# Performance work log

Measured on AMD Instinct MI355X. Metric: run time of the kernel, lower is better.

## Reference

```python
import jax, jax.numpy as jnp
import numpy as np

N_NODES = 50000
N_EDGES = 800000
N_GRAPHS = 256
W_SCALE = 0.05  # keep activations bounded through 5 relu conv layers


def setup_inputs() -> dict:
    key = jax.random.key(0)
    ks = jax.random.split(key, 16)
    rn = lambda k, shape: W_SCALE * jax.random.normal(k, shape, dtype=jnp.float32)
    return {
        "x": jax.random.normal(ks[0], (N_NODES, 336), dtype=jnp.float32),
        "edge_index": jax.random.randint(ks[1], (2, N_EDGES), 0, N_NODES, dtype=jnp.int32),
        "batch": jnp.sort(jax.random.randint(ks[2], (N_NODES,), 0, N_GRAPHS, dtype=jnp.int32)),
        "w1_rel": rn(ks[3], (100, 336)),
        "w1_root": rn(ks[4], (100, 336)),
        "b1": rn(ks[5], (100,)),
        "w_rel": rn(ks[6], (4, 100, 100)),
        "w_root": rn(ks[7], (4, 100, 100)),
        "b": rn(ks[8], (4, 100)),
        "lw1": rn(ks[9], (100, 100)),
        "lb1": rn(ks[10], (100,)),
        "lw2": rn(ks[11], (100, 100)),
        "lb2": rn(ks[12], (100,)),
        "lw3": rn(ks[13], (29, 100)),
        "lb3": rn(ks[14], (29,)),
    }


def _graph_conv(x, edge_index, w_rel, w_root, bias):
    # PyG GraphConv: out_i = W_rel @ (sum_{j->i} x_j) + b + W_root @ x_i
    src, dst = edge_index[0], edge_index[1]
    agg = jax.ops.segment_sum(x[src], dst, num_segments=x.shape[0])  # [N, d_in]
    return agg @ w_rel.T + bias + x @ w_root.T


def reference(x, edge_index, batch, w1_rel, w1_root, b1, w_rel, w_root, b,
              lw1, lb1, lw2, lb2, lw3, lb3):
    h = jax.nn.relu(_graph_conv(x, edge_index, w1_rel, w1_root, b1))  # [N,100]
    for i in range(4):  # conv2..conv5 (structurally distinct params)
        h = jax.nn.relu(_graph_conv(h, edge_index, w_rel[i], w_root[i], b[i]))
    # global_mean_pool over graphs
    sums = jax.ops.segment_sum(h, batch, num_segments=N_GRAPHS)          # [G,100]
    counts = jax.ops.segment_sum(jnp.ones((h.shape[0],), h.dtype), batch,
                                 num_segments=N_GRAPHS)                  # [G]
    pooled = sums / jnp.maximum(counts, 1.0)[:, None]
    h = jax.nn.relu(pooled @ lw1.T + lb1)
    h = jax.nn.relu(h @ lw2.T + lb2)
    return h @ lw3.T + lb3  # [G, 29]
```

## Files before the change

kernel.cpp:

```cpp
#include <hip/hip_runtime.h>

#define N_NODES 50000
#define N_EDGES 800000
#define N_GRAPHS 256
#define F 100

#define SCAN_B 512
#define SCAN_NB 98
#define SCAN_PAD (SCAN_NB * SCAN_B)

#define PART_SZ 6250
#define FILL_CHUNK 2048

typedef __attribute__((ext_vector_type(8))) short bf16x8;
typedef __attribute__((ext_vector_type(4))) float f32x4;
typedef unsigned short ushort_t;
typedef unsigned int uint_t;

__device__ inline ushort_t f2bf(float f) {
  uint_t u = __float_as_uint(f);
  uint_t r = (u + 0x7fffu + ((u >> 16) & 1u)) >> 16;
  return (ushort_t)r;
}


__global__ __launch_bounds__(256) void hist_kernel(const int* __restrict__ dst,
                                                   int* __restrict__ cnt, int E) {
  int part = blockIdx.x & 7;
  int lo = part * PART_SZ, hi = lo + PART_SZ;
  int base = (blockIdx.x >> 3) * FILL_CHUNK;
  int end = base + FILL_CHUNK; if (end > E) end = E;
  for (int i = base + threadIdx.x; i < end; i += 256) {
    int d = dst[i];
    if (d >= lo && d < hi) atomicAdd(&cnt[d], 1);
  }
}

__global__ __launch_bounds__(SCAN_B) void scan1_kernel(const int* __restrict__ cnt,
                                                       int* __restrict__ excl,
                                                       int* __restrict__ bsum) {
  __shared__ int sh[SCAN_B];
  int t = threadIdx.x;
  int i = blockIdx.x * SCAN_B + t;
  int v = cnt[i];
  sh[t] = v;
  __syncthreads();
  for (int off = 1; off < SCAN_B; off <<= 1) {
    int u = (t >= off) ? sh[t - off] : 0;
    __syncthreads();
    sh[t] += u;
    __syncthreads();
  }
  excl[i] = sh[t] - v;
  if (t == SCAN_B - 1) bsum[blockIdx.x] = sh[t];
}

__global__ __launch_bounds__(128) void scan2_kernel(int* __restrict__ bsum) {
  __shared__ int sh[128];
  int t = threadIdx.x;
  int v = (t < SCAN_NB) ? bsum[t] : 0;
  sh[t] = v;
  __syncthreads();
  for (int off = 1; off < 128; off <<= 1) {
    int u = (t >= off) ? sh[t - off] : 0;
    __syncthreads();
    sh[t] += u;
    __syncthreads();
  }
  if (t < SCAN_NB) bsum[t] = sh[t] - v;
}

__global__ __launch_bounds__(SCAN_B) void scan3_kernel(const int* __restrict__ excl,
                                                       const int* __restrict__ bsum,
                                                       int* __restrict__ offs,
                                                       int* __restrict__ cursor) {
  int i = blockIdx.x * SCAN_B + threadIdx.x;
  int v = excl[i] + bsum[blockIdx.x];
  if (i <= N_NODES) { offs[i] = v; cursor[i] = v; }
}

__global__ __launch_bounds__(256) void fill_kernel(const int* __restrict__ src,
                                                   const int* __restrict__ dst,
                                                   int* __restrict__ cursor,
                                                   int* __restrict__ csr_src, int E) {
  int part = blockIdx.x & 7;
  int lo = part * PART_SZ, hi = lo + PART_SZ;
  int base = (blockIdx.x >> 3) * FILL_CHUNK;
  int end = base + FILL_CHUNK; if (end > E) end = E;
  for (int i = base + threadIdx.x; i < end; i += 256) {
    int d = dst[i];
    if (d >= lo && d < hi) {
      int p = atomicAdd(&cursor[d], 1);
      csr_src[p] = src[i];
    }
  }
}


__global__ void pack_w1_kernel(const float* __restrict__ w1_rel, const float* __restrict__ w1_root,
                               ushort_t* __restrict__ Wp1) {
  int row = blockIdx.x;
  for (int k = threadIdx.x; k < 352; k += 128) {
    float v = 0.f;
    if (k < 336) {
      if (row < 100) v = w1_rel[row * 336 + k];
      else if (row < 200) v = w1_root[(row - 100) * 336 + k];
    }
    Wp1[(size_t)row * 352 + k] = f2bf(v);
  }
}

__global__ void pack_w_kernel(const float* __restrict__ w_rel, const float* __restrict__ w_root,
                              ushort_t* __restrict__ Wp) {
  int row = blockIdx.x;
  int l = blockIdx.y;
  int k = threadIdx.x;
  float v = 0.f;
  if (k < 100) {
    if (row < 100) v = w_rel[((size_t)l * 100 + row) * 100 + k];
    else if (row < 200) v = w_root[((size_t)l * 100 + row - 100) * 100 + k];
  }
  Wp[((size_t)l * 208 + row) * 128 + k] = f2bf(v);
}


template <bool AF32>
__global__ __launch_bounds__(256) void conv_mfma(
    const void* __restrict__ Aptr, const ushort_t* __restrict__ Wp,
    const float* __restrict__ bias,
    ushort_t* __restrict__ Zrel, ushort_t* __restrict__ Zroot, int Kp) {
  __shared__ short alds[64 * 32];
  __shared__ short blds[208 * 32];
  __shared__ float bias_s[104];

  int tid = threadIdx.x;
  int n0 = blockIdx.x * 64;
  if (tid < 100) bias_s[tid] = bias[tid];

  f32x4 acc[13];
#pragma unroll
  for (int b = 0; b < 13; ++b) acc[b] = (f32x4)0.f;

  int w = tid >> 6, lane = tid & 63, q = lane >> 4, m16 = lane & 15;

  for (int k0 = 0; k0 < Kp; k0 += 32) {
    {
      int r = tid >> 2, qq = tid & 3;
      int node = n0 + r;
      int k = k0 + qq * 8;
      bf16x8 val = (bf16x8)0;
      if (AF32) {
        if (node < N_NODES && k < 336) {
          const float* p = (const float*)Aptr + (size_t)node * 336 + k;
          float4 f0 = *(const float4*)p;
          float4 f1 = *(const float4*)(p + 4);
          val[0] = (short)f2bf(f0.x); val[1] = (short)f2bf(f0.y);
          val[2] = (short)f2bf(f0.z); val[3] = (short)f2bf(f0.w);
          val[4] = (short)f2bf(f1.x); val[5] = (short)f2bf(f1.y);
          val[6] = (short)f2bf(f1.z); val[7] = (short)f2bf(f1.w);
        }
      } else {
        if (node < N_NODES)
          val = *(const bf16x8*)((const short*)Aptr + (size_t)node * 128 + k);
      }
      *(bf16x8*)&alds[r * 32 + qq * 8] = val;
    }
    for (int c = tid; c < 832; c += 256) {
      int r = c >> 2, qq = c & 3;
      *(bf16x8*)&blds[r * 32 + qq * 8] =
          *(const bf16x8*)((const short*)Wp + (size_t)r * Kp + k0 + qq * 8);
    }
    __syncthreads();
    bf16x8 a = *(const bf16x8*)&alds[(w * 16 + m16) * 32 + q * 8];
#pragma unroll
    for (int b = 0; b < 13; ++b) {
      bf16x8 bf = *(const bf16x8*)&blds[(b * 16 + m16) * 32 + q * 8];
      acc[b] = __builtin_amdgcn_mfma_f32_16x16x32_bf16(a, bf, acc[b], 0, 0, 0);
    }
    __syncthreads();
  }

  int node_base = n0 + w * 16 + q * 4;
#pragma unroll
  for (int b = 0; b < 13; ++b) {
    int n = b * 16 + m16;
#pragma unroll
    for (int r = 0; r < 4; ++r) {
      int node = node_base + r;
      if (node >= N_NODES) continue;
      float v = acc[b][r];
      if (n < 100) {
        Zrel[(size_t)node * 100 + n] = f2bf(v);
      } else if (n < 200) {
        Zroot[(size_t)node * 100 + (n - 100)] = f2bf(v + bias_s[n - 100]);
      }
    }
  }
}


__global__ __launch_bounds__(256) void gather_bf16(
    const ushort_t* __restrict__ Zrel, const ushort_t* __restrict__ Zroot,
    const int* __restrict__ offs, const int* __restrict__ csr,
    ushort_t* __restrict__ H) {
  int node = blockIdx.x * 4 + (threadIdx.x >> 6);
  node = __builtin_amdgcn_readfirstlane(node);
  int lane = threadIdx.x & 63;
  int off = (lane < 50 ? lane : 49) * 2;

  uint_t z = *(const uint_t*)(Zroot + (size_t)node * 100 + off);
  float p0[8], p1[8];
#pragma unroll
  for (int u = 0; u < 8; ++u) { p0[u] = 0.f; p1[u] = 0.f; }
  p0[0] = __uint_as_float(z << 16);
  p1[0] = __uint_as_float(z & 0xffff0000u);

  int s = offs[node], e = offs[node + 1];
  int j = s;
  for (; j + 7 < e; j += 8) {
    uint_t zz[8];
#pragma unroll
    for (int u = 0; u < 8; ++u) {
      int idx = csr[j + u];
      zz[u] = *(const uint_t*)(Zrel + (size_t)idx * 100 + off);
    }
#pragma unroll
    for (int u = 0; u < 8; ++u) {
      p0[u] += __uint_as_float(zz[u] << 16);
      p1[u] += __uint_as_float(zz[u] & 0xffff0000u);
    }
  }
  for (; j < e; ++j) {
    int idx = csr[j];
    uint_t z0 = *(const uint_t*)(Zrel + (size_t)idx * 100 + off);
    p0[0] += __uint_as_float(z0 << 16);
    p1[0] += __uint_as_float(z0 & 0xffff0000u);
  }
  float a0 = ((p0[0] + p0[1]) + (p0[2] + p0[3])) + ((p0[4] + p0[5]) + (p0[6] + p0[7]));
  float a1 = ((p1[0] + p1[1]) + (p1[2] + p1[3])) + ((p1[4] + p1[5]) + (p1[6] + p1[7]));
  a0 = fmaxf(a0, 0.f);
  a1 = fmaxf(a1, 0.f);
  uint_t outp = (uint_t)f2bf(a0) | ((uint_t)f2bf(a1) << 16);
  if (lane >= 50) outp = 0u;
  *(uint_t*)(H + (size_t)node * 128 + lane * 2) = outp;
}


__global__ __launch_bounds__(1024) void pool_kernel(const ushort_t* __restrict__ H,
                                                    const int* __restrict__ batch,
                                                    float* __restrict__ pooled) {
  int g = blockIdx.x;
  int t = threadIdx.x;
  int lo = 0, hi = N_NODES;
  while (lo < hi) { int mid = (lo + hi) >> 1; if (batch[mid] < g) lo = mid + 1; else hi = mid; }
  int s = lo;
  hi = N_NODES;
  while (lo < hi) { int mid = (lo + hi) >> 1; if (batch[mid] <= g) lo = mid + 1; else hi = mid; }
  int e = lo;

  int row = t >> 6;
  int lane = t & 63;
  int off = (lane < 50 ? lane : 49) * 2;
  float a0 = 0.f, a1 = 0.f;
  for (int n = s + row; n < e; n += 16) {
    uint_t z = *(const uint_t*)(H + (size_t)n * 128 + off);
    a0 += __uint_as_float(z << 16);
    a1 += __uint_as_float(z & 0xffff0000u);
  }
  __shared__ float sh[16][104];
  if (lane < 50) { sh[row][lane * 2] = a0; sh[row][lane * 2 + 1] = a1; }
  __syncthreads();
  if (t < 100) {
    float acc = 0.f;
#pragma unroll
    for (int r = 0; r < 16; ++r) acc += sh[r][t];
    int cnt = e - s;
    float d = (cnt > 0) ? (float)cnt : 1.f;
    pooled[(size_t)g * F + t] = acc / d;
  }
}


__global__ void mlp_kernel(const float* __restrict__ pooled,
                           const float* __restrict__ lw1, const float* __restrict__ lb1,
                           const float* __restrict__ lw2, const float* __restrict__ lb2,
                           const float* __restrict__ lw3, const float* __restrict__ lb3,
                           float* __restrict__ out) {
  int g = blockIdx.x;
  int t = threadIdx.x;
  __shared__ float r0[F], r1[F], r2[F];
  if (t < F) r0[t] = pooled[(size_t)g * F + t];
  __syncthreads();
  if (t < F) {
    float s = lb1[t];
    for (int k = 0; k < F; ++k) s += r0[k] * lw1[t * F + k];
    r1[t] = fmaxf(s, 0.f);
  }
  __syncthreads();
  if (t < F) {
    float s = lb2[t];
    for (int k = 0; k < F; ++k) s += r1[k] * lw2[t * F + k];
    r2[t] = fmaxf(s, 0.f);
  }
  __syncthreads();
  if (t < 29) {
    float s = lb3[t];
    for (int k = 0; k < F; ++k) s += r2[k] * lw3[t * F + k];
    out[g * 29 + t] = s;
  }
}


extern "C" void kernel_launch(void* const* d_in, const int* in_sizes, int n_in,
                              void* d_out, int out_size, void* d_ws, size_t ws_size,
                              hipStream_t stream) {
  const float* x       = (const float*)d_in[0];
  const int*   ei      = (const int*)d_in[1];
  const int*   batch   = (const int*)d_in[2];
  const float* w1_rel  = (const float*)d_in[3];
  const float* w1_root = (const float*)d_in[4];
  const float* b1      = (const float*)d_in[5];
  const float* w_rel   = (const float*)d_in[6];
  const float* w_root  = (const float*)d_in[7];
  const float* bvec    = (const float*)d_in[8];
  const float* lw1     = (const float*)d_in[9];
  const float* lb1     = (const float*)d_in[10];
  const float* lw2     = (const float*)d_in[11];
  const float* lb2     = (const float*)d_in[12];
  const float* lw3     = (const float*)d_in[13];
  const float* lb3     = (const float*)d_in[14];
  float* out = (float*)d_out;

  char* ws = (char*)d_ws;
  size_t o = 0;
  auto alloc = [&](size_t bytes) { void* p = ws + o; o = (o + bytes + 511) & ~(size_t)511; return p; };
  ushort_t* H    = (ushort_t*)alloc((size_t)N_NODES * 128 * 2);
  ushort_t* Zrel = (ushort_t*)alloc((size_t)N_NODES * 100 * 2);
  ushort_t* Zroot= (ushort_t*)alloc((size_t)N_NODES * 100 * 2);
  ushort_t* Wp1  = (ushort_t*)alloc((size_t)208 * 352 * 2);
  ushort_t* Wp   = (ushort_t*)alloc((size_t)4 * 208 * 128 * 2);
  float*    pooled = (float*)alloc((size_t)N_GRAPHS * F * 4);
  int* cnt    = (int*)alloc((size_t)SCAN_PAD * 4);
  int* excl   = (int*)alloc((size_t)SCAN_PAD * 4);
  int* bsum   = (int*)alloc((size_t)128 * 4);
  int* offs   = (int*)alloc((size_t)(N_NODES + 1) * 4);
  int* cursor = (int*)alloc((size_t)(N_NODES + 1) * 4);
  int* csr    = (int*)alloc((size_t)N_EDGES * 4);

  const int E = N_EDGES;
  const int* srcv = ei;
  const int* dstv = ei + E;

  int nchunk = (E + FILL_CHUNK - 1) / FILL_CHUNK;
  hipMemsetAsync(cnt, 0, (size_t)SCAN_PAD * sizeof(int), stream);
  hist_kernel<<<nchunk * 8, 256, 0, stream>>>(dstv, cnt, E);
  scan1_kernel<<<SCAN_NB, SCAN_B, 0, stream>>>(cnt, excl, bsum);
  scan2_kernel<<<1, 128, 0, stream>>>(bsum);
  scan3_kernel<<<SCAN_NB, SCAN_B, 0, stream>>>(excl, bsum, offs, cursor);
  fill_kernel<<<nchunk * 8, 256, 0, stream>>>(srcv, dstv, cursor, csr, E);

  pack_w1_kernel<<<208, 128, 0, stream>>>(w1_rel, w1_root, Wp1);
  pack_w_kernel<<<dim3(208, 4), 128, 0, stream>>>(w_rel, w_root, Wp);

  int mmgrid = (N_NODES + 63) / 64;
  conv_mfma<true><<<mmgrid, 256, 0, stream>>>(x, Wp1, b1, Zrel, Zroot, 352);
  gather_bf16<<<N_NODES / 4, 256, 0, stream>>>(Zrel, Zroot, offs, csr, H);
  for (int l = 0; l < 4; ++l) {
    conv_mfma<false><<<mmgrid, 256, 0, stream>>>(H, Wp + (size_t)l * 208 * 128,
                                                 bvec + (size_t)l * F, Zrel, Zroot, 128);
    gather_bf16<<<N_NODES / 4, 256, 0, stream>>>(Zrel, Zroot, offs, csr, H);
  }
  pool_kernel<<<N_GRAPHS, 1024, 0, stream>>>(H, batch, pooled);
  mlp_kernel<<<N_GRAPHS, 128, 0, stream>>>(pooled, lw1, lb1, lw2, lb2, lw3, lb3, out);
}
```

Before: 475.7 us.

## Double-buffer conv GEMM K-chunks in registers, widen to 64, unroll gather by 16

The conv MFMA kernel now works on 64-wide K chunks and prefetches the next chunk's A and B tiles into registers while MFMAs run on the current LDS tile. It also pads LDS rows to 72 shorts to reduce bank conflicts, and pads the first-layer weight to K=384 to fit the new chunk size. The gather kernel issues 16 independent neighbour loads per iteration plus a 4-wide tail, to expose more memory-level parallelism. The cost is more registers, which may lower occupancy, plus some extra zero-padded K work in layer 1.

```diff
diff --git a/kernel.cpp b/kernel.cpp
--- a/kernel.cpp
+++ b/kernel.cpp
@@ -11,6 +11,8 @@
 
 #define PART_SZ 6250
 #define FILL_CHUNK 2048
+
+#define SROW 72
 
 typedef __attribute__((ext_vector_type(8))) short bf16x8;
 typedef __attribute__((ext_vector_type(4))) float f32x4;
@@ -100,13 +102,13 @@
 __global__ void pack_w1_kernel(const float* __restrict__ w1_rel, const float* __restrict__ w1_root,
                                ushort_t* __restrict__ Wp1) {
   int row = blockIdx.x;
-  for (int k = threadIdx.x; k < 352; k += 128) {
+  for (int k = threadIdx.x; k < 384; k += 128) {
     float v = 0.f;
     if (k < 336) {
       if (row < 100) v = w1_rel[row * 336 + k];
       else if (row < 200) v = w1_root[(row - 100) * 336 + k];
     }
-    Wp1[(size_t)row * 352 + k] = f2bf(v);
+    Wp1[(size_t)row * 384 + k] = f2bf(v);
   }
 }
 
@@ -129,8 +131,8 @@
     const void* __restrict__ Aptr, const ushort_t* __restrict__ Wp,
     const float* __restrict__ bias,
     ushort_t* __restrict__ Zrel, ushort_t* __restrict__ Zroot, int Kp) {
-  __shared__ short alds[64 * 32];
-  __shared__ short blds[208 * 32];
+  __shared__ short alds[64 * SROW];
+  __shared__ short blds[208 * SROW];
   __shared__ float bias_s[104];
 
   int tid = threadIdx.x;
@@ -143,11 +145,17 @@
 
   int w = tid >> 6, lane = tid & 63, q = lane >> 4, m16 = lane & 15;
 
-  for (int k0 = 0; k0 < Kp; k0 += 32) {
-    {
-      int r = tid >> 2, qq = tid & 3;
-      int node = n0 + r;
-      int k = k0 + qq * 8;
+  int ar[2], aq[2];
+#pragma unroll
+  for (int u = 0; u < 2; ++u) { int c = tid + u * 256; ar[u] = c >> 3; aq[u] = c & 7; }
+
+  bf16x8 areg[2], breg[7];
+
+  auto load_chunk = [&](int k0) {
+#pragma unroll
+    for (int u = 0; u < 2; ++u) {
+      int node = n0 + ar[u];
+      int k = k0 + aq[u] * 8;
       bf16x8 val = (bf16x8)0;
       if (AF32) {
         if (node < N_NODES && k < 336) {
@@ -163,19 +171,42 @@
         if (node < N_NODES)
           val = *(const bf16x8*)((const short*)Aptr + (size_t)node * 128 + k);
       }
-      *(bf16x8*)&alds[r * 32 + qq * 8] = val;
-    }
-    for (int c = tid; c < 832; c += 256) {
-      int r = c >> 2, qq = c & 3;
-      *(bf16x8*)&blds[r * 32 + qq * 8] =
-          *(const bf16x8*)((const short*)Wp + (size_t)r * Kp + k0 + qq * 8);
-    }
-    __syncthreads();
-    bf16x8 a = *(const bf16x8*)&alds[(w * 16 + m16) * 32 + q * 8];
-#pragma unroll
-    for (int b = 0; b < 13; ++b) {
-      bf16x8 bf = *(const bf16x8*)&blds[(b * 16 + m16) * 32 + q * 8];
-      acc[b] = __builtin_amdgcn_mfma_f32_16x16x32_bf16(a, bf, acc[b], 0, 0, 0);
+      areg[u] = val;
+    }
+#pragma unroll
+    for (int u = 0; u < 7; ++u) {
+      int c = tid + u * 256;
+      if (c < 1664) {
+        int r = c >> 3, qq = c & 7;
+        breg[u] = *(const bf16x8*)((const short*)Wp + (size_t)r * Kp + k0 + qq * 8);
+      }
+    }
+  };
+
+  load_chunk(0);
+
+  for (int k0 = 0; k0 < Kp; k0 += 64) {
+#pragma unroll
+    for (int u = 0; u < 2; ++u)
+      *(bf16x8*)&alds[ar[u] * SROW + aq[u] * 8] = areg[u];
+#pragma unroll
+    for (int u = 0; u < 7; ++u) {
+      int c = tid + u * 256;
+      if (c < 1664) {
+        int r = c >> 3, qq = c & 7;
+        *(bf16x8*)&blds[r * SROW + qq * 8] = breg[u];
+      }
+    }
+    __syncthreads();
+    if (k0 + 64 < Kp) load_chunk(k0 + 64);
+#pragma unroll
+    for (int s = 0; s < 2; ++s) {
+      bf16x8 a = *(const bf16x8*)&alds[(w * 16 + m16) * SROW + s * 32 + q * 8];
+#pragma unroll
+      for (int b = 0; b < 13; ++b) {
+        bf16x8 bf = *(const bf16x8*)&blds[(b * 16 + m16) * SROW + s * 32 + q * 8];
+        acc[b] = __builtin_amdgcn_mfma_f32_16x16x32_bf16(a, bf, acc[b], 0, 0, 0);
+      }
     }
     __syncthreads();
   }
@@ -217,15 +248,28 @@
 
   int s = offs[node], e = offs[node + 1];
   int j = s;
-  for (; j + 7 < e; j += 8) {
-    uint_t zz[8];
-#pragma unroll
-    for (int u = 0; u < 8; ++u) {
+  for (; j + 15 < e; j += 16) {
+    uint_t zz[16];
+#pragma unroll
+    for (int u = 0; u < 16; ++u) {
       int idx = csr[j + u];
       zz[u] = *(const uint_t*)(Zrel + (size_t)idx * 100 + off);
     }
 #pragma unroll
-    for (int u = 0; u < 8; ++u) {
+    for (int u = 0; u < 16; ++u) {
+      p0[u & 7] += __uint_as_float(zz[u] << 16);
+      p1[u & 7] += __uint_as_float(zz[u] & 0xffff0000u);
+    }
+  }
+  for (; j + 3 < e; j += 4) {
+    uint_t zz[4];
+#pragma unroll
+    for (int u = 0; u < 4; ++u) {
+      int idx = csr[j + u];
+      zz[u] = *(const uint_t*)(Zrel + (size_t)idx * 100 + off);
+    }
+#pragma unroll
+    for (int u = 0; u < 4; ++u) {
       p0[u] += __uint_as_float(zz[u] << 16);
       p1[u] += __uint_as_float(zz[u] & 0xffff0000u);
     }
@@ -337,7 +381,7 @@
   ushort_t* H    = (ushort_t*)alloc((size_t)N_NODES * 128 * 2);
   ushort_t* Zrel = (ushort_t*)alloc((size_t)N_NODES * 100 * 2);
   ushort_t* Zroot= (ushort_t*)alloc((size_t)N_NODES * 100 * 2);
-  ushort_t* Wp1  = (ushort_t*)alloc((size_t)208 * 352 * 2);
+  ushort_t* Wp1  = (ushort_t*)alloc((size_t)208 * 384 * 2);
   ushort_t* Wp   = (ushort_t*)alloc((size_t)4 * 208 * 128 * 2);
   float*    pooled = (float*)alloc((size_t)N_GRAPHS * F * 4);
   int* cnt    = (int*)alloc((size_t)SCAN_PAD * 4);
@@ -363,7 +407,7 @@
   pack_w_kernel<<<dim3(208, 4), 128, 0, stream>>>(w_rel, w_root, Wp);
 
   int mmgrid = (N_NODES + 63) / 64;
-  conv_mfma<true><<<mmgrid, 256, 0, stream>>>(x, Wp1, b1, Zrel, Zroot, 352);
+  conv_mfma<true><<<mmgrid, 256, 0, stream>>>(x, Wp1, b1, Zrel, Zroot, 384);
   gather_bf16<<<N_NODES / 4, 256, 0, stream>>>(Zrel, Zroot, offs, csr, H);
   for (int l = 0; l < 4; ++l) {
     conv_mfma<false><<<mmgrid, 256, 0, stream>>>(H, Wp + (size_t)l * 208 * 128,
```

Result: no change. 468.3 us (-1.6%).

## Split conv GEMM over output halves, drop LDS staging, widen gather to 128-padded rows

Applied to the files above, without the earlier changes.

The conv GEMM now splits the 224 padded output columns into two grid halves of 112. It loads A and W fragments directly from global memory into MFMA operands, with the K loop fully unrolled, instead of staging them through LDS with barriers. Zrel and Zroot are padded to 128-element rows. The gather kernel loads a wave's 64 CSR indices at once, broadcasts them with readlane, and has each half-wave process a different neighbor with 8-byte loads, then combines the halves with a shuffle. The aim is to remove LDS and sync overhead and to raise memory-level parallelism in the edge gather. The cost is redundant global A loads across the two halves and more padded bytes.

```diff
diff --git a/kernel.cpp b/kernel.cpp
--- a/kernel.cpp
+++ b/kernel.cpp
@@ -12,6 +12,8 @@
 #define PART_SZ 6250
 #define FILL_CHUNK 2048
 
+#define NBH 112
+
 typedef __attribute__((ext_vector_type(8))) short bf16x8;
 typedef __attribute__((ext_vector_type(4))) float f32x4;
 typedef unsigned short ushort_t;
@@ -22,6 +24,8 @@
   uint_t r = (u + 0x7fffu + ((u >> 16) & 1u)) >> 16;
   return (ushort_t)r;
 }
+__device__ inline float bflo(uint_t u) { return __uint_as_float(u << 16); }
+__device__ inline float bfhi(uint_t u) { return __uint_as_float(u & 0xffff0000u); }
 
 
 __global__ __launch_bounds__(256) void hist_kernel(const int* __restrict__ dst,
@@ -120,79 +124,68 @@
     if (row < 100) v = w_rel[((size_t)l * 100 + row) * 100 + k];
     else if (row < 200) v = w_root[((size_t)l * 100 + row - 100) * 100 + k];
   }
-  Wp[((size_t)l * 208 + row) * 128 + k] = f2bf(v);
-}
-
-
-template <bool AF32>
+  Wp[((size_t)l * 224 + row) * 128 + k] = f2bf(v);
+}
+
+
+template <bool AF32, int NS>
 __global__ __launch_bounds__(256) void conv_mfma(
     const void* __restrict__ Aptr, const ushort_t* __restrict__ Wp,
     const float* __restrict__ bias,
     ushort_t* __restrict__ Zrel, ushort_t* __restrict__ Zroot, int Kp) {
-  __shared__ short alds[64 * 32];
-  __shared__ short blds[208 * 32];
-  __shared__ float bias_s[104];
-
   int tid = threadIdx.x;
+  int w = tid >> 6, lane = tid & 63, q = lane >> 4, m16 = lane & 15;
   int n0 = blockIdx.x * 64;
-  if (tid < 100) bias_s[tid] = bias[tid];
-
-  f32x4 acc[13];
-#pragma unroll
-  for (int b = 0; b < 13; ++b) acc[b] = (f32x4)0.f;
-
-  int w = tid >> 6, lane = tid & 63, q = lane >> 4, m16 = lane & 15;
-
-  for (int k0 = 0; k0 < Kp; k0 += 32) {
-    {
-      int r = tid >> 2, qq = tid & 3;
-      int node = n0 + r;
-      int k = k0 + qq * 8;
+  int h = blockIdx.y;
+  int arow = n0 + w * 16 + m16;
+  int arow_c = arow < N_NODES ? arow : N_NODES - 1;
+
+  f32x4 acc[7];
+#pragma unroll
+  for (int b = 0; b < 7; ++b) acc[b] = (f32x4)0.f;
+
+  const ushort_t* wbase = Wp + (size_t)(h * NBH) * Kp;
+
+#pragma unroll
+  for (int s = 0; s < NS; ++s) {
+    int base = s * 32 + q * 8;
+    bf16x8 a;
+    if (AF32) {
       bf16x8 val = (bf16x8)0;
-      if (AF32) {
-        if (node < N_NODES && k < 336) {
-          const float* p = (const float*)Aptr + (size_t)node * 336 + k;
-          float4 f0 = *(const float4*)p;
-          float4 f1 = *(const float4*)(p + 4);
-          val[0] = (short)f2bf(f0.x); val[1] = (short)f2bf(f0.y);
-          val[2] = (short)f2bf(f0.z); val[3] = (short)f2bf(f0.w);
-          val[4] = (short)f2bf(f1.x); val[5] = (short)f2bf(f1.y);
-          val[6] = (short)f2bf(f1.z); val[7] = (short)f2bf(f1.w);
-        }
-      } else {
-        if (node < N_NODES)
-          val = *(const bf16x8*)((const short*)Aptr + (size_t)node * 128 + k);
+      if (base < 336) {
+        const float* p = (const float*)Aptr + (size_t)arow_c * 336 + base;
+        float4 f0 = *(const float4*)p;
+        float4 f1 = *(const float4*)(p + 4);
+        val[0] = (short)f2bf(f0.x); val[1] = (short)f2bf(f0.y);
+        val[2] = (short)f2bf(f0.z); val[3] = (short)f2bf(f0.w);
+        val[4] = (short)f2bf(f1.x); val[5] = (short)f2bf(f1.y);
+        val[6] = (short)f2bf(f1.z); val[7] = (short)f2bf(f1.w);
       }
-      *(bf16x8*)&alds[r * 32 + qq * 8] = val;
-    }
-    for (int c = tid; c < 832; c += 256) {
-      int r = c >> 2, qq = c & 3;
-      *(bf16x8*)&blds[r * 32 + qq * 8] =
-          *(const bf16x8*)((const short*)Wp + (size_t)r * Kp + k0 + qq * 8);
-    }
-    __syncthreads();
-    bf16x8 a = *(const bf16x8*)&alds[(w * 16 + m16) * 32 + q * 8];
-#pragma unroll
-    for (int b = 0; b < 13; ++b) {
-      bf16x8 bf = *(const bf16x8*)&blds[(b * 16 + m16) * 32 + q * 8];
+      a = val;
+    } else {
+      a = *(const bf16x8*)((const ushort_t*)Aptr + (size_t)arow_c * 128 + base);
+    }
+#pragma unroll
+    for (int b = 0; b < 7; ++b) {
+      bf16x8 bf = *(const bf16x8*)(wbase + (size_t)(b * 16 + m16) * Kp + base);
       acc[b] = __builtin_amdgcn_mfma_f32_16x16x32_bf16(a, bf, acc[b], 0, 0, 0);
     }
-    __syncthreads();
   }
 
   int node_base = n0 + w * 16 + q * 4;
 #pragma unroll
-  for (int b = 0; b < 13; ++b) {
-    int n = b * 16 + m16;
+  for (int b = 0; b < 7; ++b) {
+    int n = h * NBH + b * 16 + m16;
+    float bv = (n >= 100 && n < 200) ? bias[n - 100] : 0.f;
 #pragma unroll
     for (int r = 0; r < 4; ++r) {
       int node = node_base + r;
       if (node >= N_NODES) continue;
       float v = acc[b][r];
       if (n < 100) {
-        Zrel[(size_t)node * 100 + n] = f2bf(v);
+        Zrel[(size_t)node * 128 + n] = f2bf(v);
       } else if (n < 200) {
-        Zroot[(size_t)node * 100 + (n - 100)] = f2bf(v + bias_s[n - 100]);
+        Zroot[(size_t)node * 128 + (n - 100)] = f2bf(v + bv);
       }
     }
   }
@@ -206,43 +199,61 @@
   int node = blockIdx.x * 4 + (threadIdx.x >> 6);
   node = __builtin_amdgcn_readfirstlane(node);
   int lane = threadIdx.x & 63;
-  int off = (lane < 50 ? lane : 49) * 2;
-
-  uint_t z = *(const uint_t*)(Zroot + (size_t)node * 100 + off);
-  float p0[8], p1[8];
-#pragma unroll
-  for (int u = 0; u < 8; ++u) { p0[u] = 0.f; p1[u] = 0.f; }
-  p0[0] = __uint_as_float(z << 16);
-  p1[0] = __uint_as_float(z & 0xffff0000u);
+  int half = lane >> 5;
+  int sl = lane & 31;
+
+  float a0[4], a1[4], a2[4], a3[4];
+#pragma unroll
+  for (int c = 0; c < 4; ++c) { a0[c] = 0.f; a1[c] = 0.f; a2[c] = 0.f; a3[c] = 0.f; }
+  if (half == 0) {
+    uint2 z = *(const uint2*)(Zroot + (size_t)node * 128 + sl * 4);
+    a0[0] = bflo(z.x); a0[1] = bfhi(z.x); a0[2] = bflo(z.y); a0[3] = bfhi(z.y);
+  }
 
   int s = offs[node], e = offs[node + 1];
-  int j = s;
-  for (; j + 7 < e; j += 8) {
-    uint_t zz[8];
-#pragma unroll
-    for (int u = 0; u < 8; ++u) {
-      int idx = csr[j + u];
-      zz[u] = *(const uint_t*)(Zrel + (size_t)idx * 100 + off);
-    }
-#pragma unroll
-    for (int u = 0; u < 8; ++u) {
-      p0[u] += __uint_as_float(zz[u] << 16);
-      p1[u] += __uint_as_float(zz[u] & 0xffff0000u);
-    }
-  }
-  for (; j < e; ++j) {
-    int idx = csr[j];
-    uint_t z0 = *(const uint_t*)(Zrel + (size_t)idx * 100 + off);
-    p0[0] += __uint_as_float(z0 << 16);
-    p1[0] += __uint_as_float(z0 & 0xffff0000u);
-  }
-  float a0 = ((p0[0] + p0[1]) + (p0[2] + p0[3])) + ((p0[4] + p0[5]) + (p0[6] + p0[7]));
-  float a1 = ((p1[0] + p1[1]) + (p1[2] + p1[3])) + ((p1[4] + p1[5]) + (p1[6] + p1[7]));
-  a0 = fmaxf(a0, 0.f);
-  a1 = fmaxf(a1, 0.f);
-  uint_t outp = (uint_t)f2bf(a0) | ((uint_t)f2bf(a1) << 16);
-  if (lane >= 50) outp = 0u;
-  *(uint_t*)(H + (size_t)node * 128 + lane * 2) = outp;
+  for (int j = s; j < e; j += 64) {
+    int take = e - j; if (take > 64) take = 64;
+    int vidx = (lane < take) ? csr[j + lane] : 0;
+    int u = 0;
+    for (; u + 8 <= take; u += 8) {
+      int idxp[4];
+#pragma unroll
+      for (int p = 0; p < 4; ++p) {
+        int iA = __builtin_amdgcn_readlane(vidx, u + 2 * p);
+        int iB = __builtin_amdgcn_readlane(vidx, u + 2 * p + 1);
+        idxp[p] = half ? iB : iA;
+      }
+      uint2 v[4];
+#pragma unroll
+      for (int p = 0; p < 4; ++p)
+        v[p] = *(const uint2*)(Zrel + (size_t)idxp[p] * 128 + sl * 4);
+      a0[0] += bflo(v[0].x); a0[1] += bfhi(v[0].x); a0[2] += bflo(v[0].y); a0[3] += bfhi(v[0].y);
+      a1[0] += bflo(v[1].x); a1[1] += bfhi(v[1].x); a1[2] += bflo(v[1].y); a1[3] += bfhi(v[1].y);
+      a2[0] += bflo(v[2].x); a2[1] += bfhi(v[2].x); a2[2] += bflo(v[2].y); a2[3] += bfhi(v[2].y);
+      a3[0] += bflo(v[3].x); a3[1] += bfhi(v[3].x); a3[2] += bflo(v[3].y); a3[3] += bfhi(v[3].y);
+    }
+    for (; u < take; u += 2) {
+      int iA = __builtin_amdgcn_readlane(vidx, u);
+      int iB = (u + 1 < take) ? __builtin_amdgcn_readlane(vidx, u + 1) : iA;
+      int idx = half ? iB : iA;
+      uint2 v = *(const uint2*)(Zrel + (size_t)idx * 128 + sl * 4);
+      if (u + half >= take) { v.x = 0u; v.y = 0u; }
+      a0[0] += bflo(v.x); a0[1] += bfhi(v.x); a0[2] += bflo(v.y); a0[3] += bfhi(v.y);
+    }
+  }
+
+#pragma unroll
+  for (int c = 0; c < 4; ++c) {
+    float t = (a0[c] + a1[c]) + (a2[c] + a3[c]);
+    t += __shfl_xor(t, 32, 64);
+    a0[c] = fmaxf(t, 0.f);
+  }
+  if (half == 0) {
+    uint2 outp;
+    outp.x = (uint_t)f2bf(a0[0]) | ((uint_t)f2bf(a0[1]) << 16);
+    outp.y = (uint_t)f2bf(a0[2]) | ((uint_t)f2bf(a0[3]) << 16);
+    *(uint2*)(H + (size_t)node * 128 + sl * 4) = outp;
+  }
 }
 
 
@@ -264,8 +275,8 @@
   float a0 = 0.f, a1 = 0.f;
   for (int n = s + row; n < e; n += 16) {
     uint_t z = *(const uint_t*)(H + (size_t)n * 128 + off);
-    a0 += __uint_as_float(z << 16);
-    a1 += __uint_as_float(z & 0xffff0000u);
+    a0 += bflo(z);
+    a1 += bfhi(z);
   }
   __shared__ float sh[16][104];
   if (lane < 50) { sh[row][lane * 2] = a0; sh[row][lane * 2 + 1] = a1; }
@@ -335,10 +346,10 @@
   size_t o = 0;
   auto alloc = [&](size_t bytes) { void* p = ws + o; o = (o + bytes + 511) & ~(size_t)511; return p; };
   ushort_t* H    = (ushort_t*)alloc((size_t)N_NODES * 128 * 2);
-  ushort_t* Zrel = (ushort_t*)alloc((size_t)N_NODES * 100 * 2);
-  ushort_t* Zroot= (ushort_t*)alloc((size_t)N_NODES * 100 * 2);
-  ushort_t* Wp1  = (ushort_t*)alloc((size_t)208 * 352 * 2);
-  ushort_t* Wp   = (ushort_t*)alloc((size_t)4 * 208 * 128 * 2);
+  ushort_t* Zrel = (ushort_t*)alloc((size_t)N_NODES * 128 * 2);
+  ushort_t* Zroot= (ushort_t*)alloc((size_t)N_NODES * 128 * 2);
+  ushort_t* Wp1  = (ushort_t*)alloc((size_t)224 * 352 * 2);
+  ushort_t* Wp   = (ushort_t*)alloc((size_t)4 * 224 * 128 * 2);
   float*    pooled = (float*)alloc((size_t)N_GRAPHS * F * 4);
   int* cnt    = (int*)alloc((size_t)SCAN_PAD * 4);
   int* excl   = (int*)alloc((size_t)SCAN_PAD * 4);
@@ -359,15 +370,15 @@
   scan3_kernel<<<SCAN_NB, SCAN_B, 0, stream>>>(excl, bsum, offs, cursor);
   fill_kernel<<<nchunk * 8, 256, 0, stream>>>(srcv, dstv, cursor, csr, E);
 
-  pack_w1_kernel<<<208, 128, 0, stream>>>(w1_rel, w1_root, Wp1);
-  pack_w_kernel<<<dim3(208, 4), 128, 0, stream>>>(w_rel, w_root, Wp);
-
-  int mmgrid = (N_NODES + 63) / 64;
-  conv_mfma<true><<<mmgrid, 256, 0, stream>>>(x, Wp1, b1, Zrel, Zroot, 352);
+  pack_w1_kernel<<<224, 128, 0, stream>>>(w1_rel, w1_root, Wp1);
+  pack_w_kernel<<<dim3(224, 4), 128, 0, stream>>>(w_rel, w_root, Wp);
+
+  dim3 mmgrid((N_NODES + 63) / 64, 2);
+  conv_mfma<true, 11><<<mmgrid, 256, 0, stream>>>(x, Wp1, b1, Zrel, Zroot, 352);
   gather_bf16<<<N_NODES / 4, 256, 0, stream>>>(Zrel, Zroot, offs, csr, H);
   for (int l = 0; l < 4; ++l) {
-    conv_mfma<false><<<mmgrid, 256, 0, stream>>>(H, Wp + (size_t)l * 208 * 128,
-                                                 bvec + (size_t)l * F, Zrel, Zroot, 128);
+    conv_mfma<false, 4><<<mmgrid, 256, 0, stream>>>(H, Wp + (size_t)l * 224 * 128,
+                                                    bvec + (size_t)l * F, Zrel, Zroot, 128);
     gather_bf16<<<N_NODES / 4, 256, 0, stream>>>(Zrel, Zroot, offs, csr, H);
   }
   pool_kernel<<<N_GRAPHS, 1024, 0, stream>>>(H, batch, pooled);
```

Measured after the change: 562.3 us. +18.2%, slower.
